# Kernel tuning notes

Hardware: AMD Instinct MI355X
Metric: run time of the kernel (lower is better)

## Reference

```python
import jax, jax.numpy as jnp
import numpy as np

T, H, E, I, K, G, KG = 16384, 1024, 64, 768, 8, 8, 4


def setup_inputs() -> dict:
    key = jax.random.key(0)
    ks = jax.random.split(key, 6)
    return {
        "hidden_states": jax.random.normal(ks[0], (T, H), jnp.float32),
        "gate_weight": jax.random.normal(ks[1], (E, H), jnp.float32) * 0.02,
        "correction_bias": jax.random.normal(ks[2], (E,), jnp.float32) * 0.01,
        "w_gate": jax.random.normal(ks[3], (E, I, H), jnp.float32) * 0.02,
        "w_up": jax.random.normal(ks[4], (E, I, H), jnp.float32) * 0.02,
        "w_down": jax.random.normal(ks[5], (E, H, I), jnp.float32) * 0.02,
    }


def _grouped_topk(hidden, gate_w, bias, top_k=K, n_group=G, topk_group=KG, renormalize=True):
    # gate runs in fp32 (MoEGate.dtype = float32)
    logits = hidden.astype(jnp.float32) @ gate_w.T  # [T, E]
    scores = jax.nn.sigmoid(logits)  # noaux_tc uses sigmoid scores
    s_choice = scores + bias[None, :].astype(jnp.float32)
    t, e = scores.shape
    # group score = sum of top-2 biased scores within each group
    grouped = s_choice.reshape(t, n_group, e // n_group)
    top2, _ = jax.lax.top_k(grouped, 2)
    group_scores = top2.sum(-1)  # [T, G]
    _, gidx = jax.lax.top_k(group_scores, topk_group)  # [T, KG]
    gmask = jnp.zeros((t, n_group), jnp.float32).at[jnp.arange(t)[:, None], gidx].set(1.0)
    emask = jnp.repeat(gmask, e // n_group, axis=1)  # [T, E]
    masked = jnp.where(emask > 0, s_choice, -jnp.inf)
    _, topk_idx = jax.lax.top_k(masked, top_k)  # [T, K]
    # weights use the unbiased sigmoid scores
    topk_w = jnp.take_along_axis(scores, topk_idx, axis=1)
    if renormalize:
        topk_w = topk_w / (topk_w.sum(-1, keepdims=True) + 1e-20)
    # routed_scaling_factor = 1.0
    return topk_idx, topk_w


def reference(hidden_states, gate_weight, correction_bias, w_gate, w_up, w_down):
    t = hidden_states.shape[0]
    topk_idx, topk_w = _grouped_topk(hidden_states, gate_weight, correction_bias)
    # dense combine weights [T, E]: zero except at selected experts
    combine = jnp.zeros((t, E), hidden_states.dtype).at[
        jnp.arange(t)[:, None], topk_idx
    ].add(topk_w.astype(hidden_states.dtype))

    def step(acc, xs):
        wg, wu, wd, c = xs  # wg/wu: [I,H], wd: [H,I], c: [T]
        h = jax.nn.silu(hidden_states @ wg.T) * (hidden_states @ wu.T)  # [T, I]
        return acc + c[:, None] * (h @ wd.T), None

    acc0 = jnp.zeros_like(hidden_states)
    out, _ = jax.lax.scan(step, acc0, (w_gate, w_up, w_down, combine.T))
    return out
```

## Files before the change

kernel.cpp:

```cpp
#include <hip/hip_runtime.h>
#include <hip/hip_bf16.h>
#include <math.h>

#define T_TOK 16384
#define H_DIM 1024
#define E_NUM 64
#define I_DIM 768
#define TOPK  8
#define NGRP  8
#define KGRP  4
#define S_ASN (T_TOK*TOPK)
#define BM 128
#define BK 64
#define MAXBLK (S_ASN/BM + E_NUM)

typedef __attribute__((ext_vector_type(4))) float f4v;
typedef __attribute__((ext_vector_type(8))) short s8v;

#define GLDS16(g, l) __builtin_amdgcn_global_load_lds( \
    (const __attribute__((address_space(1))) void*)(g), \
    (__attribute__((address_space(3))) void*)(l), 16, 0, 0)

static __device__ __forceinline__ short f2bf(float f){
  union { float f; unsigned u; } a; a.f = f;
  unsigned u = a.u;
  unsigned r = (u + 0x7fffu + ((u >> 16) & 1u)) >> 16;
  return (short)r;
}
static __device__ __forceinline__ s8v cvt8(f4v a, f4v b){
  s8v r;
  r[0]=f2bf(a[0]); r[1]=f2bf(a[1]); r[2]=f2bf(a[2]); r[3]=f2bf(a[3]);
  r[4]=f2bf(b[0]); r[5]=f2bf(b[1]); r[6]=f2bf(b[2]); r[7]=f2bf(b[3]);
  return r;
}

__launch_bounds__(256)
__global__ void cast_kernel(const float* __restrict__ src,
                            short* __restrict__ dst, long n8)
{
  long i = (long)blockIdx.x*blockDim.x + threadIdx.x;
  long stride = (long)gridDim.x*blockDim.x;
  for (; i < n8; i += stride){
    f4v a = *(const f4v*)(src + i*8);
    f4v b = *(const f4v*)(src + i*8 + 4);
    *(s8v*)(dst + i*8) = cvt8(a, b);
  }
}

__launch_bounds__(256)
__global__ void gate_kernel(const float* __restrict__ hidden,
                            const float* __restrict__ gate_w,
                            double* __restrict__ logits)
{
  __shared__ float sX[64][33];
  __shared__ float sW[64][33];
  const int tid  = threadIdx.x;
  const int t0   = blockIdx.x * 64;
  const int srow = tid >> 2;
  const int scol = (tid & 3) * 8;
  const int tx = tid & 15, ty = tid >> 4;
  double acc[4][4];
  #pragma unroll
  for (int i=0;i<4;i++)
    #pragma unroll
    for (int j=0;j<4;j++) acc[i][j]=0.0;

  for (int k0=0;k0<H_DIM;k0+=32){
    f4v a0 = *(const f4v*)&hidden[(size_t)(t0+srow)*H_DIM + k0 + scol];
    f4v a1 = *(const f4v*)&hidden[(size_t)(t0+srow)*H_DIM + k0 + scol + 4];
    f4v b0 = *(const f4v*)&gate_w[(size_t)srow*H_DIM + k0 + scol];
    f4v b1 = *(const f4v*)&gate_w[(size_t)srow*H_DIM + k0 + scol + 4];
    __syncthreads();
    #pragma unroll
    for (int j=0;j<4;j++){
      sX[srow][scol+j]   = a0[j];  sX[srow][scol+4+j] = a1[j];
      sW[srow][scol+j]   = b0[j];  sW[srow][scol+4+j] = b1[j];
    }
    __syncthreads();
    #pragma unroll
    for (int kk=0;kk<32;kk++){
      float xv[4], wv[4];
      #pragma unroll
      for (int i=0;i<4;i++){ xv[i]=sX[ty*4+i][kk]; wv[i]=sW[tx*4+i][kk]; }
      #pragma unroll
      for (int i=0;i<4;i++)
        #pragma unroll
        for (int j=0;j<4;j++)
          acc[i][j] += (double)xv[i] * (double)wv[j];
    }
  }
  #pragma unroll
  for (int i=0;i<4;i++)
    #pragma unroll
    for (int j=0;j<4;j++)
      logits[(size_t)(t0+ty*4+i)*E_NUM + tx*4+j] = acc[i][j];
}

__global__ void route_kernel(const double* __restrict__ logits,
                             const float*  __restrict__ bias,
                             int*   __restrict__ topk_idx,
                             float* __restrict__ topk_w,
                             int*   __restrict__ counts)
{
  const int t = blockIdx.x * blockDim.x + threadIdx.x;
  if (t >= T_TOK) return;
  const double* lg = logits + (size_t)t * E_NUM;
  double sc[E_NUM], sch[E_NUM];
  for (int e2=0;e2<E_NUM;e2++){
    double s = 1.0 / (1.0 + exp(-lg[e2]));
    sc[e2]  = s;
    sch[e2] = s + (double)bias[e2];
  }
  double gs[NGRP];
  for (int g=0;g<NGRP;g++){
    double m1=-1e300, m2=-1e300;
    for (int j=0;j<8;j++){
      double v = sch[g*8+j];
      if (v > m1){ m2 = m1; m1 = v; } else if (v > m2){ m2 = v; }
    }
    gs[g] = m1 + m2;
  }
  unsigned gsel = 0;
  for (int r=0;r<KGRP;r++){
    int best = 0; double bv = -1.0e308;
    for (int g=0;g<NGRP;g++)
      if (!((gsel>>g)&1u) && gs[g] > bv){ bv = gs[g]; best = g; }
    gsel |= 1u << best;
  }
  unsigned long long used = 0ULL;
  double wsum = 0.0;
  int sel[TOPK]; double w[TOPK];
  for (int r=0;r<TOPK;r++){
    int best = 0; double bv = -1.0e308;
    for (int e2=0;e2<E_NUM;e2++){
      if ((used>>e2)&1ULL) continue;
      if (!((gsel>>(e2>>3))&1u)) continue;
      if (sch[e2] > bv){ bv = sch[e2]; best = e2; }
    }
    used |= 1ULL << best;
    sel[r] = best;
    w[r]   = sc[best];
    wsum  += w[r];
  }
  double inv = 1.0 / (wsum + 1e-20);
  for (int r=0;r<TOPK;r++){
    topk_idx[(size_t)t*TOPK + r] = sel[r];
    topk_w  [(size_t)t*TOPK + r] = (float)(w[r]*inv);
    atomicAdd(&counts[sel[r]], 1);
  }
}

__global__ void scan_kernel(const int* __restrict__ counts,
                            int* __restrict__ offsets,
                            int* __restrict__ blk_start)
{
  if (threadIdx.x == 0 && blockIdx.x == 0){
    int off = 0, blk = 0;
    for (int e=0;e<E_NUM;e++){
      offsets[e] = off; blk_start[e] = blk;
      off += counts[e];
      blk += (counts[e] + BM - 1) / BM;
    }
    offsets[E_NUM] = off; blk_start[E_NUM] = blk;
  }
}

__global__ void scatter_kernel(const int* __restrict__ topk_idx,
                               const float* __restrict__ topk_w,
                               const int* __restrict__ offsets,
                               int* __restrict__ cursor,
                               int* __restrict__ token_list,
                               float* __restrict__ weight_list)
{
  const int t = blockIdx.x*blockDim.x + threadIdx.x;
  if (t >= T_TOK) return;
  for (int r=0;r<TOPK;r++){
    int   e2 = topk_idx[(size_t)t*TOPK + r];
    float wv = topk_w [(size_t)t*TOPK + r];
    int p = atomicAdd(&cursor[e2], 1);
    token_list [offsets[e2] + p] = t;
    weight_list[offsets[e2] + p] = wv;
  }
}


__launch_bounds__(512, 4)
__global__ void ffn1_fast(const short* __restrict__ hid_bf,
                          const short* __restrict__ wg_bf,
                          const short* __restrict__ wu_bf,
                          const int*   __restrict__ token_list,
                          const float* __restrict__ weight_list,
                          const int*   __restrict__ offsets,
                          const int*   __restrict__ blk_start,
                          short*       __restrict__ h_all)
{
  __shared__ short lsX[128*64];
  __shared__ short lsG[128*64];
  __shared__ short lsU[128*64];
  __shared__ float lsWt[128];

  const int bx = blockIdx.x;
  if (bx >= blk_start[E_NUM]) return;
  int e = 0;
  while (blk_start[e+1] <= bx) ++e;
  const int rb   = bx - blk_start[e];
  const int cb   = blockIdx.y;
  const int base = offsets[e];
  const int n_e  = offsets[e+1] - base;
  const int row0 = rb * BM;

  const int tid = threadIdx.x;
  const int lane = tid & 63, wid = tid >> 6;
  const int wm = wid >> 2, wn = wid & 3;
  const int l15 = lane & 15, l4 = lane >> 4;

  if (tid < BM) lsWt[tid] = ((row0+tid) < n_e) ? weight_list[base+row0+tid] : 0.f;

  const short* srcA[2];
  #pragma unroll
  for (int i=0;i<2;i++){
    int s_lin = i*512 + tid;
    int row = s_lin >> 3, sl = s_lin & 7;
    int asn = base + row0 + row; if (asn >= S_ASN) asn = S_ASN-1;
    int tok = token_list[asn];
    srcA[i] = hid_bf + (size_t)tok*H_DIM + ((sl ^ (row&7))<<3);
  }
  const short* srcG[2]; const short* srcU[2];
  #pragma unroll
  for (int i=0;i<2;i++){
    int s_lin = i*512 + tid;
    int row = s_lin >> 3, sl = s_lin & 7;
    size_t wrow = ((size_t)e*I_DIM + cb*128 + row)*H_DIM + ((sl ^ (row&7))<<3);
    srcG[i] = wg_bf + wrow;
    srcU[i] = wu_bf + wrow;
  }
  short* dstA0 = lsX + wid*512;
  short* dstG0 = lsG + wid*512;
  short* dstU0 = lsU + wid*512;

  f4v accg[4][2], accu[4][2];
  #pragma unroll
  for (int m=0;m<4;m++)
    #pragma unroll
    for (int n=0;n<2;n++){
      accg[m][n]=(f4v){0.f,0.f,0.f,0.f};
      accu[m][n]=(f4v){0.f,0.f,0.f,0.f};
    }

  for (int k0=0; k0<H_DIM; k0+=BK){
    __syncthreads();
    #pragma unroll
    for (int i=0;i<2;i++) GLDS16(srcA[i]+k0, dstA0 + i*4096);
    #pragma unroll
    for (int i=0;i<2;i++) GLDS16(srcG[i]+k0, dstG0 + i*4096);
    #pragma unroll
    for (int i=0;i<2;i++) GLDS16(srcU[i]+k0, dstU0 + i*4096);
    __syncthreads();
    #pragma unroll
    for (int kk=0;kk<2;kk++){
      s8v af[4], bg[2], bu[2];
      #pragma unroll
      for (int m=0;m<4;m++){
        int r = wm*64 + m*16 + l15;
        int s = (kk*4 + l4) ^ (r & 7);
        af[m] = *(const s8v*)&lsX[r*64 + (s<<3)];
      }
      #pragma unroll
      for (int n=0;n<2;n++){
        int r = wn*32 + n*16 + l15;
        int s = (kk*4 + l4) ^ (r & 7);
        bg[n] = *(const s8v*)&lsG[r*64 + (s<<3)];
        bu[n] = *(const s8v*)&lsU[r*64 + (s<<3)];
      }
      #pragma unroll
      for (int m=0;m<4;m++)
        #pragma unroll
        for (int n=0;n<2;n++){
          accg[m][n] = __builtin_amdgcn_mfma_f32_16x16x32_bf16(af[m], bg[n], accg[m][n], 0,0,0);
          accu[m][n] = __builtin_amdgcn_mfma_f32_16x16x32_bf16(af[m], bu[n], accu[m][n], 0,0,0);
        }
    }
  }
  #pragma unroll
  for (int m=0;m<4;m++){
    #pragma unroll
    for (int i=0;i<4;i++){
      int r = wm*64 + m*16 + l4*4 + i;
      if (row0 + r < n_e){
        float wgt = lsWt[r];
        size_t hb = (size_t)(base+row0+r)*I_DIM + (size_t)cb*128;
        #pragma unroll
        for (int n=0;n<2;n++){
          int c = wn*32 + n*16 + l15;
          float g = accg[m][n][i], u = accu[m][n][i];
          float s = g / (1.f + __expf(-g));
          h_all[hb + c] = f2bf(s * u * wgt);
        }
      }
    }
  }
}

__launch_bounds__(256, 3)
__global__ void ffn2_fast(const short* __restrict__ h_all,
                          const short* __restrict__ wd_bf,
                          const int*   __restrict__ token_list,
                          const int*   __restrict__ offsets,
                          const int*   __restrict__ blk_start,
                          float*       __restrict__ out)
{
  __shared__ short lsA[128*64];
  __shared__ short lsB[128*64];
  __shared__ int   lsT[128];

  const int bx = blockIdx.x;
  if (bx >= blk_start[E_NUM]) return;
  int e = 0;
  while (blk_start[e+1] <= bx) ++e;
  const int rb   = bx - blk_start[e];
  const int cb   = blockIdx.y;
  const int base = offsets[e];
  const int n_e  = offsets[e+1] - base;
  const int row0 = rb * BM;

  const int tid = threadIdx.x;
  const int lane = tid & 63, wid = tid >> 6;
  const int wm = wid >> 1, wn = wid & 1;
  const int l15 = lane & 15, l4 = lane >> 4;

  if (tid < BM) lsT[tid] = ((row0+tid) < n_e) ? token_list[base+row0+tid] : -1;

  const short* srcA[4]; const short* srcB[4];
  #pragma unroll
  for (int i=0;i<4;i++){
    int s_lin = i*256 + tid;
    int row = s_lin >> 3, sl = s_lin & 7;
    int arow = base + row0 + row; if (arow >= S_ASN) arow = S_ASN-1;
    srcA[i] = h_all + (size_t)arow*I_DIM + ((sl ^ (row&7))<<3);
    srcB[i] = wd_bf + ((size_t)e*H_DIM + cb*128 + row)*I_DIM + ((sl ^ (row&7))<<3);
  }
  short* dstA0 = lsA + wid*512;
  short* dstB0 = lsB + wid*512;

  f4v acc[4][4];
  #pragma unroll
  for (int m=0;m<4;m++)
    #pragma unroll
    for (int n=0;n<4;n++) acc[m][n]=(f4v){0.f,0.f,0.f,0.f};

  for (int k0=0; k0<I_DIM; k0+=BK){
    __syncthreads();
    #pragma unroll
    for (int i=0;i<4;i++) GLDS16(srcA[i]+k0, dstA0 + i*2048);
    #pragma unroll
    for (int i=0;i<4;i++) GLDS16(srcB[i]+k0, dstB0 + i*2048);
    __syncthreads();
    #pragma unroll
    for (int kk=0;kk<2;kk++){
      s8v af[4], bf[4];
      #pragma unroll
      for (int m=0;m<4;m++){
        int r = wm*64 + m*16 + l15;
        int s = (kk*4 + l4) ^ (r & 7);
        af[m] = *(const s8v*)&lsA[r*64 + (s<<3)];
      }
      #pragma unroll
      for (int n=0;n<4;n++){
        int r = wn*64 + n*16 + l15;
        int s = (kk*4 + l4) ^ (r & 7);
        bf[n] = *(const s8v*)&lsB[r*64 + (s<<3)];
      }
      #pragma unroll
      for (int m=0;m<4;m++)
        #pragma unroll
        for (int n=0;n<4;n++)
          acc[m][n] = __builtin_amdgcn_mfma_f32_16x16x32_bf16(af[m], bf[n], acc[m][n], 0,0,0);
    }
  }
  #pragma unroll
  for (int m=0;m<4;m++){
    #pragma unroll
    for (int i=0;i<4;i++){
      int r = wm*64 + m*16 + l4*4 + i;
      int tk = lsT[r];
      if (tk >= 0){
        #pragma unroll
        for (int n=0;n<4;n++){
          int c = cb*128 + wn*64 + n*16 + l15;
          atomicAdd(&out[(size_t)tk*H_DIM + c], acc[m][n][i]);
        }
      }
    }
  }
}

__launch_bounds__(512, 2)
__global__ void ffn1_kernel(const float* __restrict__ hidden,
                            const float* __restrict__ w_gate,
                            const float* __restrict__ w_up,
                            const int*   __restrict__ token_list,
                            const float* __restrict__ weight_list,
                            const int*   __restrict__ offsets,
                            const int*   __restrict__ blk_start,
                            short*       __restrict__ h_all)
{
  __shared__ short lsX[BM*64];
  __shared__ short lsG[BM*64];
  __shared__ short lsU[BM*64];
  __shared__ float lsWt[BM];

  const int bx = blockIdx.x;
  if (bx >= blk_start[E_NUM]) return;
  int e = 0;
  while (blk_start[e+1] <= bx) ++e;
  const int rb   = bx - blk_start[e];
  const int cb   = blockIdx.y;
  const int base = offsets[e];
  const int n_e  = offsets[e+1] - base;
  const int row0 = rb * BM;

  const int tid   = threadIdx.x;
  const int srow  = tid >> 2;
  const int scol  = (tid & 3) << 4;
  const int slot0 = (tid & 3) << 1;
  const int wsl0  = srow*64 + (((slot0  ) ^ (srow & 7)) << 3);
  const int wsl1  = srow*64 + (((slot0+1) ^ (srow & 7)) << 3);

  const bool tvalid = (row0 + srow) < n_e;
  int tok = 0;
  if (tvalid) tok = token_list[base + row0 + srow];
  const float* xsrc = hidden + (size_t)tok * H_DIM + scol;
  const size_t woff = (size_t)e * I_DIM * H_DIM + (size_t)(cb*128 + srow) * H_DIM + scol;
  const float* gsrc = w_gate + woff;
  const float* usrc = w_up   + woff;

  const int lane = tid & 63, wid = tid >> 6;
  const int wm = wid >> 2, wn = wid & 3;
  const int l15 = lane & 15, l4 = lane >> 4;

  f4v accg[4][2], accu[4][2];
  #pragma unroll
  for (int m=0;m<4;m++)
    #pragma unroll
    for (int n=0;n<2;n++){
      accg[m][n]=(f4v){0.f,0.f,0.f,0.f};
      accu[m][n]=(f4v){0.f,0.f,0.f,0.f};
    }

  for (int k0=0; k0<H_DIM; k0+=BK){
    f4v x0,x1,x2,x3;
    if (tvalid){
      x0 = *(const f4v*)(xsrc+k0);   x1 = *(const f4v*)(xsrc+k0+4);
      x2 = *(const f4v*)(xsrc+k0+8); x3 = *(const f4v*)(xsrc+k0+12);
    } else {
      x0=x1=x2=x3=(f4v){0.f,0.f,0.f,0.f};
    }
    f4v g0 = *(const f4v*)(gsrc+k0),   g1 = *(const f4v*)(gsrc+k0+4);
    f4v g2 = *(const f4v*)(gsrc+k0+8), g3 = *(const f4v*)(gsrc+k0+12);
    f4v u0 = *(const f4v*)(usrc+k0),   u1 = *(const f4v*)(usrc+k0+4);
    f4v u2 = *(const f4v*)(usrc+k0+8), u3 = *(const f4v*)(usrc+k0+12);
    __syncthreads();
    *(s8v*)&lsX[wsl0] = cvt8(x0,x1);  *(s8v*)&lsX[wsl1] = cvt8(x2,x3);
    *(s8v*)&lsG[wsl0] = cvt8(g0,g1);  *(s8v*)&lsG[wsl1] = cvt8(g2,g3);
    *(s8v*)&lsU[wsl0] = cvt8(u0,u1);  *(s8v*)&lsU[wsl1] = cvt8(u2,u3);
    __syncthreads();
    #pragma unroll
    for (int kk=0;kk<2;kk++){
      s8v af[4], bg[2], bu[2];
      #pragma unroll
      for (int m=0;m<4;m++){
        int r = wm*64 + m*16 + l15;
        int s = (kk*4 + l4) ^ (r & 7);
        af[m] = *(const s8v*)&lsX[r*64 + (s<<3)];
      }
      #pragma unroll
      for (int n=0;n<2;n++){
        int r = wn*32 + n*16 + l15;
        int s = (kk*4 + l4) ^ (r & 7);
        bg[n] = *(const s8v*)&lsG[r*64 + (s<<3)];
        bu[n] = *(const s8v*)&lsU[r*64 + (s<<3)];
      }
      #pragma unroll
      for (int m=0;m<4;m++)
        #pragma unroll
        for (int n=0;n<2;n++){
          accg[m][n] = __builtin_amdgcn_mfma_f32_16x16x32_bf16(af[m], bg[n], accg[m][n], 0,0,0);
          accu[m][n] = __builtin_amdgcn_mfma_f32_16x16x32_bf16(af[m], bu[n], accu[m][n], 0,0,0);
        }
    }
  }
  if (tid < BM) lsWt[tid] = ((row0+tid) < n_e) ? weight_list[base+row0+tid] : 0.f;
  __syncthreads();
  #pragma unroll
  for (int m=0;m<4;m++){
    #pragma unroll
    for (int i=0;i<4;i++){
      int r = wm*64 + m*16 + l4*4 + i;
      if (row0 + r < n_e){
        float wgt = lsWt[r];
        size_t hb = (size_t)(base+row0+r)*I_DIM + (size_t)cb*128;
        #pragma unroll
        for (int n=0;n<2;n++){
          int c = wn*32 + n*16 + l15;
          float g = accg[m][n][i], u = accu[m][n][i];
          float s = g / (1.f + __expf(-g));
          h_all[hb + c] = f2bf(s * u * wgt);
        }
      }
    }
  }
}

__launch_bounds__(512, 2)
__global__ void ffn2_kernel(const short* __restrict__ h_all,
                            const float* __restrict__ w_down,
                            const int*   __restrict__ token_list,
                            const int*   __restrict__ offsets,
                            const int*   __restrict__ blk_start,
                            float*       __restrict__ out)
{
  __shared__ short lsA[BM*64];
  __shared__ short lsB[BM*64];
  __shared__ int   lsT[BM];

  const int bx = blockIdx.x;
  if (bx >= blk_start[E_NUM]) return;
  int e = 0;
  while (blk_start[e+1] <= bx) ++e;
  const int rb   = bx - blk_start[e];
  const int cb   = blockIdx.y;
  const int base = offsets[e];
  const int n_e  = offsets[e+1] - base;
  const int row0 = rb * BM;

  const int tid   = threadIdx.x;
  const int srow  = tid >> 2;
  const int slot0 = (tid & 3) << 1;
  const int wsl0  = srow*64 + (((slot0  ) ^ (srow & 7)) << 3);
  const int wsl1  = srow*64 + (((slot0+1) ^ (srow & 7)) << 3);

  int arow = base + row0 + srow;
  if (arow >= S_ASN) arow = S_ASN - 1;
  const short* asrc = h_all + (size_t)arow*I_DIM + ((tid&3)<<4);
  const float* bsrc = w_down + (size_t)e*H_DIM*I_DIM
                    + (size_t)(cb*128 + srow)*I_DIM + ((tid&3)<<4);

  const int lane = tid & 63, wid = tid >> 6;
  const int wm = wid >> 2, wn = wid & 3;
  const int l15 = lane & 15, l4 = lane >> 4;

  f4v acc[4][2];
  #pragma unroll
  for (int m=0;m<4;m++)
    #pragma unroll
    for (int n=0;n<2;n++) acc[m][n]=(f4v){0.f,0.f,0.f,0.f};

  for (int k0=0; k0<I_DIM; k0+=BK){
    s8v alo = *(const s8v*)(asrc + k0);
    s8v ahi = *(const s8v*)(asrc + k0 + 8);
    f4v b0 = *(const f4v*)(bsrc+k0),   b1 = *(const f4v*)(bsrc+k0+4);
    f4v b2 = *(const f4v*)(bsrc+k0+8), b3 = *(const f4v*)(bsrc+k0+12);
    __syncthreads();
    *(s8v*)&lsA[wsl0] = alo;          *(s8v*)&lsA[wsl1] = ahi;
    *(s8v*)&lsB[wsl0] = cvt8(b0,b1);  *(s8v*)&lsB[wsl1] = cvt8(b2,b3);
    __syncthreads();
    #pragma unroll
    for (int kk=0;kk<2;kk++){
      s8v af[4], bf[2];
      #pragma unroll
      for (int m=0;m<4;m++){
        int r = wm*64 + m*16 + l15;
        int s = (kk*4 + l4) ^ (r & 7);
        af[m] = *(const s8v*)&lsA[r*64 + (s<<3)];
      }
      #pragma unroll
      for (int n=0;n<2;n++){
        int r = wn*32 + n*16 + l15;
        int s = (kk*4 + l4) ^ (r & 7);
        bf[n] = *(const s8v*)&lsB[r*64 + (s<<3)];
      }
      #pragma unroll
      for (int m=0;m<4;m++)
        #pragma unroll
        for (int n=0;n<2;n++)
          acc[m][n] = __builtin_amdgcn_mfma_f32_16x16x32_bf16(af[m], bf[n], acc[m][n], 0,0,0);
    }
  }
  if (tid < BM) lsT[tid] = ((row0+tid) < n_e) ? token_list[base+row0+tid] : -1;
  __syncthreads();
  #pragma unroll
  for (int m=0;m<4;m++){
    #pragma unroll
    for (int i=0;i<4;i++){
      int r = wm*64 + m*16 + l4*4 + i;
      int tk = lsT[r];
      if (tk >= 0){
        #pragma unroll
        for (int n=0;n<2;n++){
          int c = cb*128 + wn*32 + n*16 + l15;
          atomicAdd(&out[(size_t)tk*H_DIM + c], acc[m][n][i]);
        }
      }
    }
  }
}

extern "C" void kernel_launch(void* const* d_in, const int* in_sizes, int n_in,
                              void* d_out, int out_size, void* d_ws, size_t ws_size,
                              hipStream_t stream)
{
  const float* hidden = (const float*)d_in[0];
  const float* gate_w = (const float*)d_in[1];
  const float* bias   = (const float*)d_in[2];
  const float* w_gate = (const float*)d_in[3];
  const float* w_up   = (const float*)d_in[4];
  const float* w_down = (const float*)d_in[5];
  float* out = (float*)d_out;

  char* ws = (char*)d_ws;
  size_t off = 0;
  #define WALLOC(bytes) (ws + off); off += (((size_t)(bytes)) + 255) & ~(size_t)255
  double* logits    = (double*)WALLOC((size_t)T_TOK*E_NUM*8);
  int*    topk_idx  = (int*)   WALLOC((size_t)T_TOK*TOPK*4);
  float*  topk_w    = (float*) WALLOC((size_t)T_TOK*TOPK*4);
  int*    counts    = (int*)   WALLOC(256);
  int*    cursor    = (int*)   WALLOC(256);
  int*    offsets   = (int*)   WALLOC(512);
  int*    blk_st    = (int*)   WALLOC(512);
  int*    token_l   = (int*)   WALLOC((size_t)S_ASN*4);
  float*  weight_l  = (float*) WALLOC((size_t)S_ASN*4);
  short*  h_all     = (short*) WALLOC((size_t)S_ASN*I_DIM*2);
  const size_t base_need = off;
  short*  hid_bf    = (short*) WALLOC((size_t)T_TOK*H_DIM*2);
  short*  wg_bf     = (short*) WALLOC((size_t)E_NUM*I_DIM*H_DIM*2);
  short*  wu_bf     = (short*) WALLOC((size_t)E_NUM*I_DIM*H_DIM*2);
  short*  wd_bf     = (short*) WALLOC((size_t)E_NUM*H_DIM*I_DIM*2);
  const size_t fast_need = off;
  #undef WALLOC

  const bool fast = (ws_size >= fast_need);
  if (ws_size < base_need) return;

  hipMemsetAsync(counts, 0, 512, stream);
  hipMemsetAsync(out, 0, (size_t)T_TOK*H_DIM*4, stream);

  gate_kernel   <<<T_TOK/64,  256, 0, stream>>>(hidden, gate_w, logits);
  route_kernel  <<<T_TOK/256, 256, 0, stream>>>(logits, bias, topk_idx, topk_w, counts);
  scan_kernel   <<<1, 64, 0, stream>>>(counts, offsets, blk_st);
  scatter_kernel<<<T_TOK/256, 256, 0, stream>>>(topk_idx, topk_w, offsets, cursor,
                                                token_l, weight_l);
  if (fast){
    long n8h = (long)T_TOK*H_DIM/8;
    long n8w = (long)E_NUM*I_DIM*H_DIM/8;
    cast_kernel<<<2048, 256, 0, stream>>>(hidden, hid_bf, n8h);
    cast_kernel<<<2048, 256, 0, stream>>>(w_gate, wg_bf, n8w);
    cast_kernel<<<2048, 256, 0, stream>>>(w_up,   wu_bf, n8w);
    cast_kernel<<<2048, 256, 0, stream>>>(w_down, wd_bf, n8w);
    dim3 g1(MAXBLK, I_DIM/128);
    ffn1_fast<<<g1, 512, 0, stream>>>(hid_bf, wg_bf, wu_bf, token_l, weight_l,
                                      offsets, blk_st, h_all);
    dim3 g2(MAXBLK, H_DIM/128);
    ffn2_fast<<<g2, 256, 0, stream>>>(h_all, wd_bf, token_l, offsets, blk_st, out);
  } else {
    dim3 g1(MAXBLK, I_DIM/128);
    ffn1_kernel<<<g1, 512, 0, stream>>>(hidden, w_gate, w_up, token_l, weight_l,
                                        offsets, blk_st, h_all);
    dim3 g2(MAXBLK, H_DIM/128);
    ffn2_kernel<<<g2, 512, 0, stream>>>(h_all, w_down, token_l, offsets, blk_st, out);
  }
}
```

Baseline: 1.774 ms.

## Replace FFN2 atomic scatter with bf16 staging buffer and gather-combine pass

```diff
diff --git a/kernel.cpp b/kernel.cpp
--- a/kernel.cpp
+++ b/kernel.cpp
@@ -16,6 +16,7 @@
 
 typedef __attribute__((ext_vector_type(4))) float f4v;
 typedef __attribute__((ext_vector_type(8))) short s8v;
+typedef __attribute__((ext_vector_type(4))) unsigned short u4sv;
 
 #define GLDS16(g, l) __builtin_amdgcn_global_load_lds( \
     (const __attribute__((address_space(1))) void*)(g), \
@@ -26,6 +27,9 @@
   unsigned u = a.u;
   unsigned r = (u + 0x7fffu + ((u >> 16) & 1u)) >> 16;
   return (short)r;
+}
+static __device__ __forceinline__ float bf2f(unsigned short h){
+  union { unsigned u; float f; } a; a.u = ((unsigned)h) << 16; return a.f;
 }
 static __device__ __forceinline__ s8v cvt8(f4v a, f4v b){
   s8v r;
@@ -50,7 +54,8 @@
 __launch_bounds__(256)
 __global__ void gate_kernel(const float* __restrict__ hidden,
                             const float* __restrict__ gate_w,
-                            double* __restrict__ logits)
+                            double* __restrict__ logits,
+                            short*  __restrict__ hb)
 {
   __shared__ float sX[64][33];
   __shared__ float sW[64][33];
@@ -70,6 +75,8 @@
     f4v a1 = *(const f4v*)&hidden[(size_t)(t0+srow)*H_DIM + k0 + scol + 4];
     f4v b0 = *(const f4v*)&gate_w[(size_t)srow*H_DIM + k0 + scol];
     f4v b1 = *(const f4v*)&gate_w[(size_t)srow*H_DIM + k0 + scol + 4];
+    if (hb)
+      *(s8v*)&hb[(size_t)(t0+srow)*H_DIM + k0 + scol] = cvt8(a0, a1);
     __syncthreads();
     #pragma unroll
     for (int j=0;j<4;j++){
@@ -170,7 +177,8 @@
                                const int* __restrict__ offsets,
                                int* __restrict__ cursor,
                                int* __restrict__ token_list,
-                               float* __restrict__ weight_list)
+                               float* __restrict__ weight_list,
+                               int* __restrict__ pos_list)
 {
   const int t = blockIdx.x*blockDim.x + threadIdx.x;
   if (t >= T_TOK) return;
@@ -180,6 +188,7 @@
     int p = atomicAdd(&cursor[e2], 1);
     token_list [offsets[e2] + p] = t;
     weight_list[offsets[e2] + p] = wv;
+    pos_list[(size_t)t*TOPK + r] = offsets[e2] + p;
   }
 }
 
@@ -301,63 +310,61 @@
   }
 }
 
-__launch_bounds__(256, 3)
-__global__ void ffn2_fast(const short* __restrict__ h_all,
-                          const short* __restrict__ wd_bf,
-                          const int*   __restrict__ token_list,
-                          const int*   __restrict__ offsets,
-                          const int*   __restrict__ blk_start,
-                          float*       __restrict__ out)
+__launch_bounds__(512, 4)
+__global__ void ffn2y_fast(const short* __restrict__ h_all,
+                           const short* __restrict__ wd_bf,
+                           const int*   __restrict__ offsets,
+                           const int*   __restrict__ blk_start,
+                           short*       __restrict__ y,
+                           int          cb0)
 {
   __shared__ short lsA[128*64];
   __shared__ short lsB[128*64];
-  __shared__ int   lsT[128];
 
   const int bx = blockIdx.x;
   if (bx >= blk_start[E_NUM]) return;
   int e = 0;
   while (blk_start[e+1] <= bx) ++e;
   const int rb   = bx - blk_start[e];
-  const int cb   = blockIdx.y;
+  const int cby  = blockIdx.y;
+  const int cbg  = cb0*4 + cby;
   const int base = offsets[e];
   const int n_e  = offsets[e+1] - base;
   const int row0 = rb * BM;
 
   const int tid = threadIdx.x;
   const int lane = tid & 63, wid = tid >> 6;
-  const int wm = wid >> 1, wn = wid & 1;
+  const int wm = wid >> 2, wn = wid & 3;
   const int l15 = lane & 15, l4 = lane >> 4;
 
-  if (tid < BM) lsT[tid] = ((row0+tid) < n_e) ? token_list[base+row0+tid] : -1;
-
-  const short* srcA[4]; const short* srcB[4];
-  #pragma unroll
-  for (int i=0;i<4;i++){
-    int s_lin = i*256 + tid;
+  const short* srcA[2]; const short* srcB[2];
+  #pragma unroll
+  for (int i=0;i<2;i++){
+    int s_lin = i*512 + tid;
     int row = s_lin >> 3, sl = s_lin & 7;
     int arow = base + row0 + row; if (arow >= S_ASN) arow = S_ASN-1;
     srcA[i] = h_all + (size_t)arow*I_DIM + ((sl ^ (row&7))<<3);
-    srcB[i] = wd_bf + ((size_t)e*H_DIM + cb*128 + row)*I_DIM + ((sl ^ (row&7))<<3);
+    srcB[i] = wd_bf + ((size_t)e*H_DIM + cbg*128 + row)*I_DIM + ((sl ^ (row&7))<<3);
   }
   short* dstA0 = lsA + wid*512;
   short* dstB0 = lsB + wid*512;
 
-  f4v acc[4][4];
+  f4v acc[4][2];
   #pragma unroll
   for (int m=0;m<4;m++)
     #pragma unroll
-    for (int n=0;n<4;n++) acc[m][n]=(f4v){0.f,0.f,0.f,0.f};
+    for (int n=0;n<2;n++) acc[m][n]=(f4v){0.f,0.f,0.f,0.f};
 
   for (int k0=0; k0<I_DIM; k0+=BK){
     __syncthreads();
     #pragma unroll
-    for (int i=0;i<4;i++) GLDS16(srcA[i]+k0, dstA0 + i*2048);
-    #pragma unroll
-    for (int i=0;i<4;i++) GLDS16(srcB[i]+k0, dstB0 + i*2048);
+    for (int i=0;i<2;i++) GLDS16(srcA[i]+k0, dstA0 + i*4096);
+    #pragma unroll
+    for (int i=0;i<2;i++) GLDS16(srcB[i]+k0, dstB0 + i*4096);
     __syncthreads();
     #pragma unroll
     for (int kk=0;kk<2;kk++){
-      s8v af[4], bf[4];
+      s8v af[4], bf[2];
       #pragma unroll
       for (int m=0;m<4;m++){
         int r = wm*64 + m*16 + l15;
@@ -365,15 +372,15 @@
         af[m] = *(const s8v*)&lsA[r*64 + (s<<3)];
       }
       #pragma unroll
-      for (int n=0;n<4;n++){
-        int r = wn*64 + n*16 + l15;
+      for (int n=0;n<2;n++){
+        int r = wn*32 + n*16 + l15;
         int s = (kk*4 + l4) ^ (r & 7);
         bf[n] = *(const s8v*)&lsB[r*64 + (s<<3)];
       }
       #pragma unroll
       for (int m=0;m<4;m++)
         #pragma unroll
-        for (int n=0;n<4;n++)
+        for (int n=0;n<2;n++)
           acc[m][n] = __builtin_amdgcn_mfma_f32_16x16x32_bf16(af[m], bf[n], acc[m][n], 0,0,0);
     }
   }
@@ -382,16 +389,37 @@
     #pragma unroll
     for (int i=0;i<4;i++){
       int r = wm*64 + m*16 + l4*4 + i;
-      int tk = lsT[r];
-      if (tk >= 0){
-        #pragma unroll
-        for (int n=0;n<4;n++){
-          int c = cb*128 + wn*64 + n*16 + l15;
-          atomicAdd(&out[(size_t)tk*H_DIM + c], acc[m][n][i]);
+      if (row0 + r < n_e){
+        size_t yb = (size_t)(base+row0+r)*512 + (size_t)cby*128;
+        #pragma unroll
+        for (int n=0;n<2;n++){
+          int c = wn*32 + n*16 + l15;
+          y[yb + c] = f2bf(acc[m][n][i]);
         }
       }
     }
   }
+}
+
+__launch_bounds__(256)
+__global__ void combine_kernel(const short* __restrict__ y,
+                               const int*   __restrict__ pos,
+                               float*       __restrict__ out,
+                               int cb0)
+{
+  const int tid = threadIdx.x;
+  const int t = blockIdx.x*2 + (tid >> 7);
+  const int c = (tid & 127) * 4;
+  const int* pp = pos + (size_t)t*TOPK;
+  float s0=0.f, s1=0.f, s2=0.f, s3=0.f;
+  #pragma unroll
+  for (int r=0;r<TOPK;r++){
+    int row = pp[r];
+    u4sv v = *(const u4sv*)&y[(size_t)row*512 + c];
+    s0 += bf2f(v[0]); s1 += bf2f(v[1]); s2 += bf2f(v[2]); s3 += bf2f(v[3]);
+  }
+  f4v o = {s0,s1,s2,s3};
+  *(f4v*)&out[(size_t)t*H_DIM + (size_t)cb0*512 + c] = o;
 }
 
 __launch_bounds__(512, 2)
@@ -629,6 +657,7 @@
   int*    blk_st    = (int*)   WALLOC(512);
   int*    token_l   = (int*)   WALLOC((size_t)S_ASN*4);
   float*  weight_l  = (float*) WALLOC((size_t)S_ASN*4);
+  int*    pos_l     = (int*)   WALLOC((size_t)S_ASN*4);
   short*  h_all     = (short*) WALLOC((size_t)S_ASN*I_DIM*2);
   const size_t base_need = off;
   short*  hid_bf    = (short*) WALLOC((size_t)T_TOK*H_DIM*2);
@@ -637,31 +666,35 @@
   short*  wd_bf     = (short*) WALLOC((size_t)E_NUM*H_DIM*I_DIM*2);
   const size_t fast_need = off;
   #undef WALLOC
+  short* y_all = hid_bf;
 
   const bool fast = (ws_size >= fast_need);
   if (ws_size < base_need) return;
 
   hipMemsetAsync(counts, 0, 512, stream);
-  hipMemsetAsync(out, 0, (size_t)T_TOK*H_DIM*4, stream);
-
-  gate_kernel   <<<T_TOK/64,  256, 0, stream>>>(hidden, gate_w, logits);
+
+  gate_kernel   <<<T_TOK/64,  256, 0, stream>>>(hidden, gate_w, logits,
+                                                fast ? hid_bf : (short*)0);
   route_kernel  <<<T_TOK/256, 256, 0, stream>>>(logits, bias, topk_idx, topk_w, counts);
   scan_kernel   <<<1, 64, 0, stream>>>(counts, offsets, blk_st);
   scatter_kernel<<<T_TOK/256, 256, 0, stream>>>(topk_idx, topk_w, offsets, cursor,
-                                                token_l, weight_l);
+                                                token_l, weight_l, pos_l);
   if (fast){
-    long n8h = (long)T_TOK*H_DIM/8;
     long n8w = (long)E_NUM*I_DIM*H_DIM/8;
-    cast_kernel<<<2048, 256, 0, stream>>>(hidden, hid_bf, n8h);
     cast_kernel<<<2048, 256, 0, stream>>>(w_gate, wg_bf, n8w);
     cast_kernel<<<2048, 256, 0, stream>>>(w_up,   wu_bf, n8w);
     cast_kernel<<<2048, 256, 0, stream>>>(w_down, wd_bf, n8w);
     dim3 g1(MAXBLK, I_DIM/128);
     ffn1_fast<<<g1, 512, 0, stream>>>(hid_bf, wg_bf, wu_bf, token_l, weight_l,
                                       offsets, blk_st, h_all);
-    dim3 g2(MAXBLK, H_DIM/128);
-    ffn2_fast<<<g2, 256, 0, stream>>>(h_all, wd_bf, token_l, offsets, blk_st, out);
+    dim3 g2(MAXBLK, 4);
+    for (int half = 0; half < 2; ++half){
+      ffn2y_fast<<<g2, 512, 0, stream>>>(h_all, wd_bf, offsets, blk_st,
+                                         y_all, half);
+      combine_kernel<<<T_TOK/2, 256, 0, stream>>>(y_all, pos_l, out, half);
+    }
   } else {
+    hipMemsetAsync(out, 0, (size_t)T_TOK*H_DIM*4, stream);
     dim3 g1(MAXBLK, I_DIM/128);
     ffn1_kernel<<<g1, 512, 0, stream>>>(hidden, w_gate, w_up, token_l, weight_l,
                                         offsets, blk_st, h_all);
```

After: 1.751 ms. No clear change (-1.3%).
